# Optimization experiments

Hardware: AMD Instinct MI355X
Metric: run time of the kernel (lower is better)

The kernel has to match this reference:

```python
import jax, jax.numpy as jnp
import numpy as np

N, B, NPG, DEG, F = 16384, 128, 128, 8, 128
E = N * DEG
H1, C1, H2, C2, H3, C3 = 3, 128, 2, 64, 2, 32
D = H1 * C1 + H2 * C2 + C3  # 544
K = 30
ND = 2048
LAMDA = 0.8


def _gatv2(x, src, dst, Wl, Wr, att, b, h, c, concat):
    n = x.shape[0]
    xl = (x @ Wl).reshape(n, h, c)
    xr = (x @ Wr).reshape(n, h, c)
    e = jax.nn.leaky_relu(xl[src] + xr[dst], 0.2)           # [E+N, h, c]
    logit = jnp.einsum('ehc,hc->eh', e, att)
    m = jax.lax.stop_gradient(jax.ops.segment_max(logit, dst, num_segments=n))
    a = jnp.exp(logit - m[dst])
    z = jax.ops.segment_sum(a, dst, num_segments=n)
    a = a / z[dst]
    out = jax.ops.segment_sum(xl[src] * a[:, :, None], dst, num_segments=n)
    out = out.reshape(n, h * c) if concat else out.mean(axis=1)
    return out + b


def _bn(x, g, b):
    m = x.mean(0)
    v = ((x - m) ** 2).mean(0)
    return (x - m) * jax.lax.rsqrt(v + 1e-5) * g + b


def _neighbor(emb, adj, W, b, idx):
    h = emb @ W + b
    A = adj + jnp.eye(adj.shape[0], dtype=adj.dtype)
    d = jax.lax.rsqrt(A.sum(axis=1))
    h = (1.0 - LAMDA) * h + LAMDA * ((d[:, None] * A * d[None, :]) @ h)
    v = h[idx]
    return v / jnp.clip(jnp.linalg.norm(v, axis=1, keepdims=True), 1e-12)


def setup_inputs():
    key = jax.random.key(0)
    it = iter(jax.random.split(key, 48))
    def nrm(shape, s=0.05):
        return jax.random.normal(next(it), shape, jnp.float32) * s
    src = jnp.repeat(jnp.arange(N, dtype=jnp.int32), DEG)
    dst = (src // NPG) * NPG + jax.random.randint(next(it), (E,), 0, NPG, dtype=jnp.int32)
    batch = jnp.arange(N, dtype=jnp.int32) // NPG
    return dict(
        x=jax.random.normal(next(it), (N, F), jnp.float32),
        edge_src=src, edge_dst=dst, batch=batch,
        pairs1=jax.random.randint(next(it), (B,), 0, ND, dtype=jnp.int32),
        pairs2=jax.random.randint(next(it), (B,), 0, ND, dtype=jnp.int32),
        drug_adj=(jax.random.uniform(next(it), (ND, ND)) < 0.01).astype(jnp.float32),
        drug_emb=jax.random.normal(next(it), (ND, ND), jnp.float32) * 0.1,
        dis_adj=(jax.random.uniform(next(it), (ND, ND)) < 0.01).astype(jnp.float32),
        dis_emb=jax.random.normal(next(it), (ND, ND), jnp.float32) * 0.1,
        Wde=nrm((ND, 32)), bde=jnp.zeros((32,), jnp.float32),
        Wse=nrm((ND, 32)), bse=jnp.zeros((32,), jnp.float32),
        W1l=nrm((F, H1 * C1)), W1r=nrm((F, H1 * C1)), att1=nrm((H1, C1)), b1=jnp.zeros((H1 * C1,), jnp.float32),
        W2l=nrm((H1 * C1, H2 * C2)), W2r=nrm((H1 * C1, H2 * C2)), att2=nrm((H2, C2)), b2=jnp.zeros((H2 * C2,), jnp.float32),
        W3l=nrm((H2 * C2, H3 * C3)), W3r=nrm((H2 * C2, H3 * C3)), att3=nrm((H3, C3)), b3=jnp.zeros((C3,), jnp.float32),
        g1=jnp.ones((H1 * C1,), jnp.float32), be1=jnp.zeros((H1 * C1,), jnp.float32),
        g2=jnp.ones((H2 * C2,), jnp.float32), be2=jnp.zeros((H2 * C2,), jnp.float32),
        Ws=nrm((D, K)), bs=jnp.zeros((K,), jnp.float32),
        Wg=nrm((D, D)), bg=jnp.zeros((D,), jnp.float32),
        Wl1=nrm((D * K + 64, 128)), bl1=jnp.zeros((128,), jnp.float32),
        Wl2=nrm((128, 1)), bl2=jnp.zeros((1,), jnp.float32),
    )


def _forward(x, drug_adj, drug_emb, dis_adj, dis_emb, Wde, bde, Wse, bse,
             W1l, W1r, att1, b1, W2l, W2r, att2, b2, W3l, W3r, att3, b3,
             g1, be1, g2, be2, Ws, bs, Wg, bg, Wl1, bl1, Wl2, bl2,
             edge_src, edge_dst, batch, pairs1, pairs2):
    loop = jnp.arange(N, dtype=edge_src.dtype)  # GATv2 self loops
    src = jnp.concatenate([edge_src, loop])
    dst = jnp.concatenate([edge_dst, loop])
    x1 = _bn(jax.nn.relu(_gatv2(x, src, dst, W1l, W1r, att1, b1, H1, C1, True)), g1, be1)
    x2 = _bn(jax.nn.relu(_gatv2(x1, src, dst, W2l, W2r, att2, b2, H2, C2, True)), g2, be2)
    x3 = _gatv2(x2, src, dst, W3l, W3r, att3, b3, H3, C3, False)
    xc = jnp.concatenate([x1, x2, x3], axis=1)              # [N, D]
    xd = xc.reshape(B, NPG, D)                              # to_dense_batch (equal graphs)
    adj = jnp.zeros((B, NPG, NPG), xc.dtype).at[
        batch[edge_src], edge_src % NPG, edge_dst % NPG].add(1.0)
    s = jax.nn.softmax(xd @ Ws + bs, axis=-1)               # [B, NPG, K]
    xp = jnp.einsum('bnk,bnd->bkd', s, xd)                  # pooled features
    ap = jnp.einsum('bnk,bnm,bml->bkl', s, adj, s)          # pooled adjacency
    ap = ap.at[:, jnp.arange(K), jnp.arange(K)].set(1.0)    # DenseGCNConv add_loop
    dg = jax.lax.rsqrt(jnp.clip(ap.sum(-1), 1.0))
    apn = dg[:, :, None] * ap * dg[:, None, :]
    xg = jax.nn.relu(jnp.einsum('bkl,bld->bkd', apn, xp @ Wg) + bg)
    de = _neighbor(drug_emb, drug_adj, Wde, bde, pairs1)    # [B, 32]
    se = _neighbor(dis_emb, dis_adj, Wse, bse, pairs2)      # [B, 32]
    g = jnp.concatenate([de, xg.reshape(B, K * D), se], axis=-1)
    h = jax.nn.relu(g @ Wl1 + bl1)
    return (h @ Wl2 + bl2)[:, 0]


def reference(x, edge_src, edge_dst, batch, pairs1, pairs2, drug_adj, drug_emb, dis_adj, dis_emb,
              Wde, bde, Wse, bse, W1l, W1r, att1, b1, W2l, W2r, att2, b2, W3l, W3r, att3, b3,
              g1, be1, g2, be2, Ws, bs, Wg, bg, Wl1, bl1, Wl2, bl2):
    return _forward(x, drug_adj, drug_emb, dis_adj, dis_emb, Wde, bde, Wse, bse,
                    W1l, W1r, att1, b1, W2l, W2r, att2, b2, W3l, W3r, att3, b3,
                    g1, be1, g2, be2, Ws, bs, Wg, bg, Wl1, bl1, Wl2, bl2,
                    edge_src, edge_dst, batch, pairs1, pairs2)
```

## Files before the change

### kernel.cpp

```cpp
#include <hip/hip_runtime.h>
#include <math.h>

#define CDIV(a,b) (((a)+(b)-1)/(b))
#define HMIN(a,b) ((a)<(b)?(a):(b))
#define MAXD 48

typedef __attribute__((ext_vector_type(8))) short bf16x8;
typedef __attribute__((ext_vector_type(4))) float f32x4;

static __device__ inline short f2bf(float x){
  unsigned u = __float_as_uint(x);
  unsigned r = (u + 0x7fffu + ((u >> 16) & 1u)) >> 16;
  return (short)r;
}

__global__ __launch_bounds__(256)
void transpose_bf16(const float* __restrict__ B, int K, int N, short* __restrict__ Bt)
{
  __shared__ float t[32][33];
  int k0 = blockIdx.x*32, n0 = blockIdx.y*32;
  int c = threadIdx.x & 31, r8 = threadIdx.x >> 5;
  for (int rr = r8; rr < 32; rr += 8) {
    int k = k0+rr, n = n0+c;
    t[rr][c] = (k < K && n < N) ? B[(size_t)k*N + n] : 0.f;
  }
  __syncthreads();
  for (int rr = r8; rr < 32; rr += 8) {
    int n = n0+rr, k = k0+c;
    if (n < N && k < K) Bt[(size_t)n*K + k] = f2bf(t[c][rr]);
  }
}

__global__ __launch_bounds__(256)
void transpose_bf16_2(const float* __restrict__ A0, int K0, int N0, short* __restrict__ D0,
                      const float* __restrict__ A1, int K1, int N1, short* __restrict__ D1)
{
  const float* B; short* Bt; int K, N;
  if (blockIdx.z == 0) { B=A0; Bt=D0; K=K0; N=N0; } else { B=A1; Bt=D1; K=K1; N=N1; }
  int ntx = CDIV(K,32), nty = CDIV(N,32);
  int tile = blockIdx.x;
  if (tile >= ntx*nty) return;
  int k0 = (tile % ntx)*32, n0 = (tile / ntx)*32;
  __shared__ float t[32][33];
  int c = threadIdx.x & 31, r8 = threadIdx.x >> 5;
  for (int rr = r8; rr < 32; rr += 8) {
    int k = k0+rr, n = n0+c;
    t[rr][c] = (k < K && n < N) ? B[(size_t)k*N + n] : 0.f;
  }
  __syncthreads();
  for (int rr = r8; rr < 32; rr += 8) {
    int n = n0+rr, k = k0+c;
    if (n < N && k < K) Bt[(size_t)n*K + k] = f2bf(t[c][rr]);
  }
}

__global__ __launch_bounds__(256)
void gemm_mfma(const float* __restrict__ A, int lda,
               const short* __restrict__ Bt,
               float* __restrict__ C, int ldc,
               int M, int N, int K,
               const float* __restrict__ bias, int relu, int ksplit)
{
  __shared__ short As[128][40];
  __shared__ short Bs[128][40];
  const int k0 = blockIdx.z * ksplit;
  const int k1 = HMIN(k0 + ksplit, K);
  C += (size_t)blockIdx.z * (size_t)M * ldc;
  const int bm = blockIdx.x * 128, bn = blockIdx.y * 128;
  const int tid = threadIdx.x;
  const int sr = tid >> 1;
  const int sk = (tid & 1) * 16;
  const int wave = tid >> 6;
  const int wr = (wave >> 1) * 64, wc = (wave & 1) * 64;
  const int lane = tid & 63;
  const int lrow = lane & 15, lk = (lane >> 4) * 8;

  f32x4 acc[4][4];
  #pragma unroll
  for (int i=0;i<4;i++)
    #pragma unroll
    for (int j=0;j<4;j++) acc[i][j] = (f32x4){0.f,0.f,0.f,0.f};

  const bool bok = (bn + sr) < N;
  for (int kb = k0; kb < k1; kb += 32) {
    __syncthreads();
    {
      const float* ap = A + (size_t)(bm + sr)*lda + kb + sk;
      float4 v0 = *(const float4*)(ap+0);
      float4 v1 = *(const float4*)(ap+4);
      float4 v2 = *(const float4*)(ap+8);
      float4 v3 = *(const float4*)(ap+12);
      bf16x8 w0, w1;
      w0[0]=f2bf(v0.x); w0[1]=f2bf(v0.y); w0[2]=f2bf(v0.z); w0[3]=f2bf(v0.w);
      w0[4]=f2bf(v1.x); w0[5]=f2bf(v1.y); w0[6]=f2bf(v1.z); w0[7]=f2bf(v1.w);
      w1[0]=f2bf(v2.x); w1[1]=f2bf(v2.y); w1[2]=f2bf(v2.z); w1[3]=f2bf(v2.w);
      w1[4]=f2bf(v3.x); w1[5]=f2bf(v3.y); w1[6]=f2bf(v3.z); w1[7]=f2bf(v3.w);
      *(bf16x8*)&As[sr][sk]   = w0;
      *(bf16x8*)&As[sr][sk+8] = w1;
    }
    {
      bf16x8 u0 = (bf16x8){0,0,0,0,0,0,0,0}, u1 = u0;
      if (bok) {
        const short* bp = Bt + (size_t)(bn + sr)*K + kb + sk;
        u0 = *(const bf16x8*)(bp);
        u1 = *(const bf16x8*)(bp+8);
      }
      *(bf16x8*)&Bs[sr][sk]   = u0;
      *(bf16x8*)&Bs[sr][sk+8] = u1;
    }
    __syncthreads();
    bf16x8 af[4], bfr[4];
    #pragma unroll
    for (int f=0;f<4;f++) af[f]  = *(const bf16x8*)&As[wr + f*16 + lrow][lk];
    #pragma unroll
    for (int f=0;f<4;f++) bfr[f] = *(const bf16x8*)&Bs[wc + f*16 + lrow][lk];
    #pragma unroll
    for (int i=0;i<4;i++)
      #pragma unroll
      for (int j=0;j<4;j++)
        acc[i][j] = __builtin_amdgcn_mfma_f32_16x16x32_bf16(af[i], bfr[j], acc[i][j], 0, 0, 0);
  }
  const int erow = (lane >> 4) * 4;
  const int ecol = lane & 15;
  #pragma unroll
  for (int j=0;j<4;j++) {
    int gcol = bn + wc + j*16 + ecol;
    if (gcol >= N) continue;
    float bv = bias ? bias[gcol] : 0.f;
    #pragma unroll
    for (int i=0;i<4;i++) {
      int grow = bm + wr + i*16 + erow;
      #pragma unroll
      for (int r=0;r<4;r++) {
        float v = acc[i][j][r] + bv;
        if (relu) v = fmaxf(v, 0.f);
        C[(size_t)(grow + r)*ldc + gcol] = v;
      }
    }
  }
}

__global__ __launch_bounds__(256)
void skinny_gemm32(const float* __restrict__ A, int lda,
                   const float* __restrict__ B,
                   float* __restrict__ Cp, int M, int ksplit)
{
  const int m0 = blockIdx.x * 32;
  const int k0 = blockIdx.z * ksplit;
  __shared__ float As[32][68];
  __shared__ float Bs[64][36];
  float acc[4] = {0.f,0.f,0.f,0.f};
  const int r  = threadIdx.x >> 3;
  const int cg = (threadIdx.x & 7) * 4;
  for (int kb = k0; kb < k0 + ksplit; kb += 64) {
    {
      int rr = threadIdx.x >> 3, ko = (threadIdx.x & 7)*8;
      const float* ap = &A[(size_t)(m0+rr)*lda + kb + ko];
      *(float4*)&As[rr][ko]   = *(const float4*)ap;
      *(float4*)&As[rr][ko+4] = *(const float4*)(ap+4);
      int br = threadIdx.x >> 2, co = (threadIdx.x & 3)*8;
      const float* bp = &B[(size_t)(kb+br)*32 + co];
      *(float4*)&Bs[br][co]   = *(const float4*)bp;
      *(float4*)&Bs[br][co+4] = *(const float4*)(bp+4);
    }
    __syncthreads();
    #pragma unroll
    for (int kk=0; kk<64; kk+=4) {
      float4 a4 = *(const float4*)&As[r][kk];
      float4 b0 = *(const float4*)&Bs[kk  ][cg];
      float4 b1 = *(const float4*)&Bs[kk+1][cg];
      float4 b2 = *(const float4*)&Bs[kk+2][cg];
      float4 b3 = *(const float4*)&Bs[kk+3][cg];
      acc[0] += a4.x*b0.x + a4.y*b1.x + a4.z*b2.x + a4.w*b3.x;
      acc[1] += a4.x*b0.y + a4.y*b1.y + a4.z*b2.y + a4.w*b3.y;
      acc[2] += a4.x*b0.z + a4.y*b1.z + a4.z*b2.z + a4.w*b3.z;
      acc[3] += a4.x*b0.w + a4.y*b1.w + a4.z*b2.w + a4.w*b3.w;
    }
    __syncthreads();
  }
  float* cp = Cp + ((size_t)blockIdx.z*M + m0 + r)*32 + cg;
  *(float4*)cp = make_float4(acc[0],acc[1],acc[2],acc[3]);
}

__global__ void build_adj(const int* __restrict__ src, const int* __restrict__ dst,
                          int E, float* __restrict__ adj)
{
  int e = blockIdx.x*blockDim.x + threadIdx.x;
  if (e >= E) return;
  int s = src[e], d = dst[e];
  int g = s >> 7;
  atomicAdd(&adj[((size_t)g*128 + (s & 127))*128 + (d & 127)], 1.0f);
}

__global__ __launch_bounds__(1024)
void build_nbr(const int* __restrict__ dst, int epg, int shift,
               int* __restrict__ nbr, int* __restrict__ deg)
{
  __shared__ short ld[1024];
  const int g = blockIdx.x;
  for (int i = threadIdx.x; i < epg; i += 1024) ld[i] = (short)(dst[g*epg + i] & 127);
  __syncthreads();
  const int d   = threadIdx.x >> 3;
  const int seg = threadIdx.x & 7;
  const int spe = epg >> 3;
  const int i0 = seg*spe, i1 = i0 + spe;
  int cnt = 0;
  for (int i = i0; i < i1; ++i) cnt += (ld[i] == (short)d) ? 1 : 0;
  int pre = cnt;
  #pragma unroll
  for (int off=1; off<8; off<<=1) {
    int v = __shfl_up(pre, off, 8);
    if (seg >= off) pre += v;
  }
  const int base  = pre - cnt;
  const int total = __shfl(pre, 7, 8);
  if (seg == 7) deg[g*128 + d] = HMIN(total, MAXD);
  const int lbase = (g*128 + d)*MAXD;
  int w = base;
  for (int i = i0; i < i1; ++i) {
    if (ld[i] == (short)d) {
      if (w < MAXD) nbr[lbase + w] = i >> shift;
      ++w;
    }
  }
}

template<int C, int NL>
__global__ __launch_bounds__(512)
void gat_attn_sp(const float* __restrict__ XL, const float* __restrict__ XR, int ldx,
                 const float* __restrict__ att,
                 const int* __restrict__ nbr, const int* __restrict__ deg,
                 const float* __restrict__ bias, int bias_per_head,
                 float* __restrict__ out, int ldo)
{
  constexpr int SPAN = C / NL;
  constexpr int NG = 512 / NL;
  constexpr int PADC = C + 4;
  __shared__ float xls[128][PADC];
  __shared__ float A_lds[128];
  __shared__ float lgs[NG][MAXD+4];
  const int g = blockIdx.x, hh = blockIdx.y;
  const int d0 = blockIdx.z * 64;
  const int colbase = hh*C;
  const int tid = threadIdx.x;
  const int lane = tid & (NL-1);
  const int grp  = tid / NL;

  for (int idx = tid; idx < 128*(C/4); idx += 512) {
    int r = idx / (C/4), q4 = idx % (C/4);
    *(float4*)&xls[r][q4*4] =
      *(const float4*)&XL[(size_t)(g*128+r)*ldx + colbase + q4*4];
  }
  float attv[SPAN];
  #pragma unroll
  for (int j=0;j<SPAN;j++) attv[j] = att[hh*C + lane*SPAN + j];
  __syncthreads();

  for (int s = grp; s < 128; s += NG) {
    float a = 0.f;
    #pragma unroll
    for (int j4=0;j4<SPAN;j4+=4) {
      float4 xv = *(const float4*)&xls[s][lane*SPAN + j4];
      a += attv[j4+0]*xv.x + attv[j4+1]*xv.y + attv[j4+2]*xv.z + attv[j4+3]*xv.w;
    }
    #pragma unroll
    for (int t=1;t<NL;t<<=1) a += __shfl_xor(a, t, 64);
    if (lane == 0) A_lds[s] = a;
  }
  __syncthreads();

  for (int d = d0 + grp; d < d0 + 64; d += NG) {
    float xrv[SPAN];
    #pragma unroll
    for (int j4=0;j4<SPAN;j4+=4)
      *(float4*)&xrv[j4] =
        *(const float4*)&XR[(size_t)(g*128+d)*ldx + colbase + lane*SPAN + j4];
    float B = 0.f;
    #pragma unroll
    for (int j=0;j<SPAN;j++) B += attv[j]*xrv[j];
    #pragma unroll
    for (int t=1;t<NL;t<<=1) B += __shfl_xor(B, t, 64);
    const int dgn = deg[g*128+d];
    const int base = (g*128+d)*MAXD;
    float m = -1e30f;
    for (int i = 0; i <= dgn; ++i) {
      int s = (i < dgn) ? nbr[base+i] : d;
      float dot = 0.f;
      #pragma unroll
      for (int j4=0;j4<SPAN;j4+=4) {
        float4 xv = *(const float4*)&xls[s][lane*SPAN + j4];
        dot += attv[j4+0]*fabsf(xv.x + xrv[j4+0]);
        dot += attv[j4+1]*fabsf(xv.y + xrv[j4+1]);
        dot += attv[j4+2]*fabsf(xv.z + xrv[j4+2]);
        dot += attv[j4+3]*fabsf(xv.w + xrv[j4+3]);
      }
      #pragma unroll
      for (int t=1;t<NL;t<<=1) dot += __shfl_xor(dot, t, 64);
      float lg = 0.6f*(A_lds[s] + B) + 0.4f*dot;
      if (lane == 0) lgs[grp][i] = lg;
      m = fmaxf(m, lg);
    }
    float z = 0.f;
    for (int i = lane; i <= dgn; i += NL) z += __expf(lgs[grp][i] - m);
    #pragma unroll
    for (int t=1;t<NL;t<<=1) z += __shfl_xor(z, t, 64);
    const float zinv = 1.f / z;
    for (int i = lane; i <= dgn; i += NL) lgs[grp][i] = __expf(lgs[grp][i] - m) * zinv;
    float acc[SPAN];
    #pragma unroll
    for (int j=0;j<SPAN;j++) acc[j]=0.f;
    for (int i = 0; i <= dgn; ++i) {
      int s = (i < dgn) ? nbr[base+i] : d;
      float P = lgs[grp][i];
      #pragma unroll
      for (int j4=0;j4<SPAN;j4+=4) {
        float4 xv = *(const float4*)&xls[s][lane*SPAN + j4];
        acc[j4+0] += P*xv.x; acc[j4+1] += P*xv.y;
        acc[j4+2] += P*xv.z; acc[j4+3] += P*xv.w;
      }
    }
    float o[SPAN];
    #pragma unroll
    for (int j=0;j<SPAN;j++) {
      int cc = lane*SPAN + j;
      float bv = bias ? (bias_per_head ? bias[colbase+cc] : bias[cc]) : 0.f;
      o[j] = acc[j] + bv;
    }
    float* op = &out[(size_t)(g*128+d)*ldo + colbase + lane*SPAN];
    #pragma unroll
    for (int j4=0;j4<SPAN;j4+=4)
      *(float4*)&op[j4] = make_float4(o[j4],o[j4+1],o[j4+2],o[j4+3]);
  }
}

__global__ __launch_bounds__(256)
void bn_partial(const float* __restrict__ in, int HC,
                float* __restrict__ psum, float* __restrict__ psq)
{
  const int cg = blockIdx.x, rb = blockIdx.y;
  const int cl = threadIdx.x & 31;
  const int rl = threadIdx.x >> 5;
  const int col = cg*32 + cl;
  float s = 0.f, s2 = 0.f;
  for (int r = rb*512 + rl; r < (rb+1)*512; r += 8) {
    float v = fmaxf(in[(size_t)r*HC + col], 0.f);
    s += v; s2 += v*v;
  }
  __shared__ float ls[8][33], ls2[8][33];
  ls[rl][cl] = s; ls2[rl][cl] = s2;
  __syncthreads();
  if (threadIdx.x < 32) {
    float a=0.f, a2=0.f;
    for (int r=0;r<8;r++){ a += ls[r][threadIdx.x]; a2 += ls2[r][threadIdx.x]; }
    psum[rb*HC + cg*32 + threadIdx.x] = a;
    psq [rb*HC + cg*32 + threadIdx.x] = a2;
  }
}

__global__ void bn_finalize(const float* __restrict__ psum, const float* __restrict__ psq,
                            int HC, float* __restrict__ mv)
{
  int c = blockIdx.x*blockDim.x + threadIdx.x;
  if (c >= HC) return;
  float s=0.f, s2=0.f;
  for (int r=0;r<32;r++){ s += psum[r*HC+c]; s2 += psq[r*HC+c]; }
  float m = s * (1.f/16384.f);
  float v = s2 * (1.f/16384.f) - m*m;
  mv[c] = m; mv[HC+c] = v;
}

__global__ void bn_apply(const float* __restrict__ in, int HC,
                         const float* __restrict__ mv,
                         const float* __restrict__ gamma, const float* __restrict__ beta,
                         float* __restrict__ out, int ldo, int total)
{
  int i = blockIdx.x*blockDim.x + threadIdx.x;
  if (i >= total) return;
  int r = i / HC, c = i % HC;
  float v = fmaxf(in[i], 0.f);
  out[(size_t)r*ldo + c] = (v - mv[c]) * rsqrtf(mv[HC+c] + 1e-5f) * gamma[c] + beta[c];
}

__global__ void combine3(const float* __restrict__ raw, float* __restrict__ xc)
{
  int i = blockIdx.x*blockDim.x + threadIdx.x;
  if (i >= 16384*32) return;
  int r = i >> 5, c = i & 31;
  xc[(size_t)r*544 + 512 + c] = 0.5f*(raw[r*64 + c] + raw[r*64 + 32 + c]);
}

__global__ void softmax30(float* __restrict__ s, int M)
{
  int w = (blockIdx.x*blockDim.x + threadIdx.x) >> 5;
  int lane = threadIdx.x & 31;
  if (w >= M) return;
  float v = (lane < 30) ? s[(size_t)w*30 + lane] : -1e30f;
  float m = v;
  for (int t=16;t>0;t>>=1) m = fmaxf(m, __shfl_xor(m, t, 32));
  float e = (lane < 30) ? __expf(v - m) : 0.f;
  float z = e;
  for (int t=16;t>0;t>>=1) z += __shfl_xor(z, t, 32);
  if (lane < 30) s[(size_t)w*30 + lane] = e / z;
}

__global__ __launch_bounds__(256)
void xp_kernel(const float* __restrict__ s, const float* __restrict__ xc,
               float* __restrict__ xp)
{
  const int b = blockIdx.x;
  const int d = blockIdx.y*256 + threadIdx.x;
  __shared__ float sb[128][32];
  for (int idx = threadIdx.x; idx < 128*30; idx += 256) {
    int n = idx/30, k = idx%30;
    sb[n][k] = s[(size_t)(b*128+n)*30 + k];
  }
  __syncthreads();
  if (d >= 544) return;
  float acc[30];
  #pragma unroll
  for (int k=0;k<30;k++) acc[k]=0.f;
  const float* xcp = xc + (size_t)b*128*544 + d;
  for (int n=0;n<128;n++) {
    float xcv = xcp[(size_t)n*544];
    const float4* sp = (const float4*)&sb[n][0];
    #pragma unroll
    for (int q=0;q<7;q++) {
      float4 v = sp[q];
      acc[q*4+0] += v.x*xcv; acc[q*4+1] += v.y*xcv;
      acc[q*4+2] += v.z*xcv; acc[q*4+3] += v.w*xcv;
    }
    float2 v2 = *(const float2*)&sb[n][28];
    acc[28] += v2.x*xcv; acc[29] += v2.y*xcv;
  }
  #pragma unroll
  for (int k=0;k<30;k++) xp[((size_t)b*30+k)*544 + d] = acc[k];
}

__global__ __launch_bounds__(256)
void pool_adj_kernel(const float* __restrict__ adj, const float* __restrict__ s,
                     float* __restrict__ apn)
{
  const int b = blockIdx.x;
  __shared__ float sb[128][32];
  __shared__ float t1s[128][32];
  __shared__ float apb[30][31];
  __shared__ float dg[30];
  for (int idx = threadIdx.x; idx < 128*30; idx += 256) {
    int n = idx/30, k = idx%30;
    sb[n][k] = s[(size_t)(b*128+n)*30 + k];
  }
  __syncthreads();
  if (threadIdx.x < 128) {
    const int i = threadIdx.x;
    float acc[30];
    #pragma unroll
    for (int k=0;k<30;k++) acc[k]=0.f;
    const float* arow = adj + ((size_t)b*128 + i)*128;
    for (int j=0;j<128;j++) {
      float a = arow[j];
      const float4* sp = (const float4*)&sb[j][0];
      #pragma unroll
      for (int q=0;q<7;q++) {
        float4 v = sp[q];
        acc[q*4+0] += v.x*a; acc[q*4+1] += v.y*a;
        acc[q*4+2] += v.z*a; acc[q*4+3] += v.w*a;
      }
      float2 v2 = *(const float2*)&sb[j][28];
      acc[28] += v2.x*a; acc[29] += v2.y*a;
    }
    #pragma unroll
    for (int k=0;k<30;k++) t1s[i][k] = acc[k];
  }
  __syncthreads();
  for (int idx = threadIdx.x; idx < 900; idx += 256) {
    int k = idx/30, l = idx%30;
    float acc = 0.f;
    for (int n=0;n<128;n++) acc += sb[n][k]*t1s[n][l];
    apb[k][l] = (k == l) ? 1.f : acc;
  }
  __syncthreads();
  if (threadIdx.x < 30) {
    float ssum = 0.f;
    for (int l=0;l<30;l++) ssum += apb[threadIdx.x][l];
    dg[threadIdx.x] = rsqrtf(fmaxf(ssum, 1.f));
  }
  __syncthreads();
  for (int idx = threadIdx.x; idx < 900; idx += 256) {
    int k = idx/30, l = idx%30;
    apn[(size_t)b*900 + idx] = dg[k]*dg[l]*apb[k][l];
  }
}

__global__ __launch_bounds__(256)
void xg_kernel(const float* __restrict__ apn, const float* __restrict__ xpw,
               const float* __restrict__ bg, float* __restrict__ g)
{
  int b = blockIdx.x;
  __shared__ float a[30][31];
  for (int idx = threadIdx.x; idx < 900; idx += 256)
    a[idx/30][idx%30] = apn[(size_t)b*900 + idx];
  __syncthreads();
  for (int idx = threadIdx.x; idx < 30*544; idx += 256) {
    int k = idx / 544, d = idx % 544;
    float acc = 0.f;
    for (int l=0;l<30;l++) acc += a[k][l] * xpw[((size_t)b*30 + l)*544 + d];
    g[(size_t)b*16384 + 32 + k*544 + d] = fmaxf(acc + bg[d], 0.f);
  }
}

__global__ __launch_bounds__(256)
void rowsum_rsqrt(const float* __restrict__ A, int n, float* __restrict__ dinv)
{
  int r = blockIdx.x;
  float s = 0.f;
  for (int j = threadIdx.x; j < n; j += 256) s += A[(size_t)r*n + j];
  for (int m=32;m>0;m>>=1) s += __shfl_xor(s, m, 64);
  __shared__ float red[4];
  if ((threadIdx.x & 63) == 0) red[threadIdx.x >> 6] = s;
  __syncthreads();
  if (threadIdx.x == 0) dinv[r] = rsqrtf(red[0]+red[1]+red[2]+red[3] + 1.f);
}

__global__ __launch_bounds__(256)
void embed_partial(const float* __restrict__ adjM, const float* __restrict__ hW,
                   const float* __restrict__ dinv, const int* __restrict__ idx,
                   float* __restrict__ part)
{
  const int b = blockIdx.x;
  const int z = blockIdx.z;
  const int row = idx[b];
  const int c  = threadIdx.x & 31;
  const int jc = threadIdx.x >> 5;
  const int j0 = z*64;
  float u = 0.f;
  #pragma unroll
  for (int t=0;t<8;t++) {
    int j = j0 + jc + t*8;
    u += adjM[(size_t)row*2048 + j] * hW[j*32 + c] * dinv[j];
  }
  __shared__ float red[8][33];
  red[jc][c] = u;
  __syncthreads();
  if (threadIdx.x < 32) {
    float s = 0.f;
    #pragma unroll
    for (int r=0;r<8;r++) s += red[r][threadIdx.x];
    part[((size_t)z*128 + b)*32 + threadIdx.x] = s;
  }
}

__global__ void embed_final(const float* __restrict__ part, const float* __restrict__ hW,
                            const float* __restrict__ dinv, const int* __restrict__ idx,
                            float* __restrict__ g, int goff)
{
  const int b = blockIdx.x;
  const int c = threadIdx.x;
  const int row = idx[b];
  float s = 0.f;
  for (int z=0; z<32; ++z) s += part[((size_t)z*128 + b)*32 + c];
  float hw = hW[(size_t)row*32 + c];
  float dv = dinv[row];
  float h2 = 0.2f*hw + 0.8f*dv*(s + hw*dv);
  float ss = h2*h2;
  #pragma unroll
  for (int m=1;m<32;m<<=1) ss += __shfl_xor(ss, m, 32);
  float nrm = fmaxf(sqrtf(ss), 1e-12f);
  g[(size_t)b*16384 + goff + c] = h2 / nrm;
}

__global__ void reduce_parts(const float* __restrict__ part, const float* __restrict__ bias,
                             float* __restrict__ outp, int total, int nz, int ldc, int relu)
{
  int i = blockIdx.x*blockDim.x + threadIdx.x;
  if (i >= total) return;
  float s = 0.f;
  for (int p=0;p<nz;p++) s += part[(size_t)p*total + i];
  if (bias) s += bias[i % ldc];
  if (relu) s = fmaxf(s, 0.f);
  outp[i] = s;
}

__global__ void final_out(const float* __restrict__ h, const float* __restrict__ Wl2,
                          const float* __restrict__ bl2, float* __restrict__ out)
{
  int m = threadIdx.x;
  if (m >= 128) return;
  float s = 0.f;
  for (int k=0;k<128;k++) s += h[m*128 + k] * Wl2[k];
  out[m] = s + bl2[0];
}

extern "C" void kernel_launch(void* const* d_in, const int* in_sizes, int n_in,
                              void* d_out, int out_size, void* d_ws, size_t ws_size,
                              hipStream_t stream)
{
  const float* x        = (const float*)d_in[0];
  const int*   edge_src = (const int*)d_in[1];
  const int*   edge_dst = (const int*)d_in[2];
  const int*   pairs1   = (const int*)d_in[4];
  const int*   pairs2   = (const int*)d_in[5];
  const float* drug_adj = (const float*)d_in[6];
  const float* drug_emb = (const float*)d_in[7];
  const float* dis_adj  = (const float*)d_in[8];
  const float* dis_emb  = (const float*)d_in[9];
  const float* Wde = (const float*)d_in[10];
  const float* bde = (const float*)d_in[11];
  const float* Wse = (const float*)d_in[12];
  const float* bse = (const float*)d_in[13];
  const float* W1l = (const float*)d_in[14];
  const float* W1r = (const float*)d_in[15];
  const float* att1= (const float*)d_in[16];
  const float* b1  = (const float*)d_in[17];
  const float* W2l = (const float*)d_in[18];
  const float* W2r = (const float*)d_in[19];
  const float* att2= (const float*)d_in[20];
  const float* b2  = (const float*)d_in[21];
  const float* W3l = (const float*)d_in[22];
  const float* W3r = (const float*)d_in[23];
  const float* att3= (const float*)d_in[24];
  const float* b3  = (const float*)d_in[25];
  const float* g1  = (const float*)d_in[26];
  const float* be1 = (const float*)d_in[27];
  const float* g2  = (const float*)d_in[28];
  const float* be2 = (const float*)d_in[29];
  const float* Wsm = (const float*)d_in[30];
  const float* bs  = (const float*)d_in[31];
  const float* Wg  = (const float*)d_in[32];
  const float* bg  = (const float*)d_in[33];
  const float* Wl1 = (const float*)d_in[34];
  const float* bl1 = (const float*)d_in[35];
  const float* Wl2 = (const float*)d_in[36];
  const float* bl2 = (const float*)d_in[37];
  float* out = (float*)d_out;

  const int E = in_sizes[1];
  const int epg = E >> 7;
  const int shift = 31 - __builtin_clz(epg >> 7);

  float* ws  = (float*)d_ws;
  float* adj = ws;
  int*   nbr = (int*)adj;
  int*   degb= nbr + 16384*MAXD;
  float* xc  = ws + 2097152;
  float* P   = ws + 11010048;
  float* XLR = P;
  float* RAW = P + 12582912;
  float* bnp = ws + 29884416;
  float* bnq = bnp + 12288;
  float* mv  = bnq + 12288;
  short* wT  = (short*)(mv + 1024);
  float* sbuf = P;
  float* xp   = P + 491520;
  float* apn  = P + 3187200;
  float* xpw  = P + 3302400;
  float* gbuf = P + 5391360;
  float* hWd  = P + 7488512;
  float* dinvd= hWd + 65536;
  float* hWs_ = dinvd + 2048;
  float* dinvs= hWs_ + 65536;
  float* upart= dinvs + 2048;
  float* partials = upart + 131072;
  float* hfin = partials + 1048576;
  float* epart = hfin + 16384;
  short* wgT  = (short*)epart;
  short* wl1T = (short*)RAW;

  build_nbr<<<128, 1024, 0, stream>>>(edge_dst, epg, shift, nbr, degb);

  transpose_bf16_2<<<dim3(48,1,2), 256, 0, stream>>>(W1l, 128, 384, wT,
                                                     W1r, 128, 384, wT + 384*128);
  gemm_mfma<<<dim3(128,6,1), 256, 0, stream>>>(x, 128, wT, XLR, 768, 16384, 768, 128, nullptr, 0, 128);
  gat_attn_sp<128,16><<<dim3(128,3,2), 512, 0, stream>>>(XLR, XLR + 384, 768, att1, nbr, degb, b1, 1, RAW, 384);
  bn_partial<<<dim3(12,32), 256, 0, stream>>>(RAW, 384, bnp, bnq);
  bn_finalize<<<2, 256, 0, stream>>>(bnp, bnq, 384, mv);
  bn_apply<<<CDIV(16384*384,256), 256, 0, stream>>>(RAW, 384, mv, g1, be1, xc, 544, 16384*384);

  transpose_bf16_2<<<dim3(48,1,2), 256, 0, stream>>>(W2l, 384, 128, wT,
                                                     W2r, 384, 128, wT + 128*384);
  gemm_mfma<<<dim3(128,2,1), 256, 0, stream>>>(xc, 544, wT, XLR, 256, 16384, 256, 384, nullptr, 0, 384);
  gat_attn_sp<64,8><<<dim3(128,2,2), 512, 0, stream>>>(XLR, XLR + 128, 256, att2, nbr, degb, b2, 1, RAW, 128);
  bn_partial<<<dim3(4,32), 256, 0, stream>>>(RAW, 128, bnp, bnq);
  bn_finalize<<<1, 256, 0, stream>>>(bnp, bnq, 128, mv);
  bn_apply<<<CDIV(16384*128,256), 256, 0, stream>>>(RAW, 128, mv, g2, be2, xc + 384, 544, 16384*128);

  transpose_bf16_2<<<dim3(8,1,2), 256, 0, stream>>>(W3l, 128, 64, wT,
                                                    W3r, 128, 64, wT + 64*128);
  gemm_mfma<<<dim3(128,1,1), 256, 0, stream>>>(xc + 384, 544, wT, XLR, 128, 16384, 128, 128, nullptr, 0, 128);
  gat_attn_sp<32,8><<<dim3(128,2,2), 512, 0, stream>>>(XLR, XLR + 64, 128, att3, nbr, degb, b3, 0, RAW, 64);
  combine3<<<CDIV(16384*32,256), 256, 0, stream>>>(RAW, xc);

  hipMemsetAsync(adj, 0, (size_t)2097152*4, stream);
  build_adj<<<CDIV(E,256), 256, 0, stream>>>(edge_src, edge_dst, E, adj);

  transpose_bf16_2<<<dim3(289,1,2), 256, 0, stream>>>(Wsm, 544, 30, wT,
                                                      Wg, 544, 544, wgT);
  gemm_mfma<<<dim3(128,1,1), 256, 0, stream>>>(xc, 544, wT, sbuf, 30, 16384, 30, 544, bs, 0, 544);
  softmax30<<<CDIV(16384*32,256), 256, 0, stream>>>(sbuf, 16384);
  xp_kernel<<<dim3(128,3), 256, 0, stream>>>(sbuf, xc, xp);
  pool_adj_kernel<<<128, 256, 0, stream>>>(adj, sbuf, apn);
  gemm_mfma<<<dim3(30,5,1), 256, 0, stream>>>(xp, 544, wgT, xpw, 544, 3840, 544, 544, nullptr, 0, 544);
  xg_kernel<<<128, 256, 0, stream>>>(apn, xpw, bg, gbuf);

  skinny_gemm32<<<dim3(64,1,8), 256, 0, stream>>>(drug_emb, 2048, Wde, epart, 2048, 256);
  reduce_parts<<<CDIV(65536,256), 256, 0, stream>>>(epart, bde, hWd, 65536, 8, 32, 0);
  rowsum_rsqrt<<<2048, 256, 0, stream>>>(drug_adj, 2048, dinvd);
  embed_partial<<<dim3(128,1,32), 256, 0, stream>>>(drug_adj, hWd, dinvd, pairs1, upart);
  embed_final<<<128, 32, 0, stream>>>(upart, hWd, dinvd, pairs1, gbuf, 0);

  skinny_gemm32<<<dim3(64,1,8), 256, 0, stream>>>(dis_emb, 2048, Wse, epart, 2048, 256);
  reduce_parts<<<CDIV(65536,256), 256, 0, stream>>>(epart, bse, hWs_, 65536, 8, 32, 0);
  rowsum_rsqrt<<<2048, 256, 0, stream>>>(dis_adj, 2048, dinvs);
  embed_partial<<<dim3(128,1,32), 256, 0, stream>>>(dis_adj, hWs_, dinvs, pairs2, upart);
  embed_final<<<128, 32, 0, stream>>>(upart, hWs_, dinvs, pairs2, gbuf, 16352);

  transpose_bf16<<<dim3(512,4), 256, 0, stream>>>(Wl1, 16384, 128, wl1T);
  gemm_mfma<<<dim3(1,1,32), 256, 0, stream>>>(gbuf, 16384, wl1T, partials, 128, 128, 128, 16384, nullptr, 0, 512);
  reduce_parts<<<CDIV(16384,256), 256, 0, stream>>>(partials, bl1, hfin, 16384, 32, 128, 1);
  final_out<<<1, 128, 0, stream>>>(hfin, Wl2, bl2, out);
}
```

Measured before the change: 485.8 us.

## Store GAT source features as bf16 in LDS, vectorize BN apply, deepen split-K

The GAT attention kernel now keeps its staged XL tile in shared memory as bf16 instead of fp32. This halves LDS footprint and read bandwidth, at some cost in numeric precision. The BN apply kernel is rewritten to process four elements per thread with float4 loads and stores. The final large-K GEMM split goes from 32 to 64 partitions, which adds parallelism but makes the partial buffer and reduction larger.

```diff
diff --git a/kernel.cpp b/kernel.cpp
--- a/kernel.cpp
+++ b/kernel.cpp
@@ -12,6 +12,9 @@
   unsigned u = __float_as_uint(x);
   unsigned r = (u + 0x7fffu + ((u >> 16) & 1u)) >> 16;
   return (short)r;
+}
+static __device__ inline float bf2f(short s){
+  return __uint_as_float(((unsigned)(unsigned short)s) << 16);
 }
 
 __global__ __launch_bounds__(256)
@@ -235,8 +238,8 @@
 {
   constexpr int SPAN = C / NL;
   constexpr int NG = 512 / NL;
-  constexpr int PADC = C + 4;
-  __shared__ float xls[128][PADC];
+  constexpr int PADC = C + 8;
+  __shared__ short xls[128][PADC];
   __shared__ float A_lds[128];
   __shared__ float lgs[NG][MAXD+4];
   const int g = blockIdx.x, hh = blockIdx.y;
@@ -246,10 +249,12 @@
   const int lane = tid & (NL-1);
   const int grp  = tid / NL;
 
-  for (int idx = tid; idx < 128*(C/4); idx += 512) {
+  for (int idx = tid; idx < 128*C/4; idx += 512) {
     int r = idx / (C/4), q4 = idx % (C/4);
-    *(float4*)&xls[r][q4*4] =
-      *(const float4*)&XL[(size_t)(g*128+r)*ldx + colbase + q4*4];
+    float4 v = *(const float4*)&XL[(size_t)(g*128+r)*ldx + colbase + q4*4];
+    short4 w;
+    w.x = f2bf(v.x); w.y = f2bf(v.y); w.z = f2bf(v.z); w.w = f2bf(v.w);
+    *(short4*)&xls[r][q4*4] = w;
   }
   float attv[SPAN];
   #pragma unroll
@@ -260,8 +265,9 @@
     float a = 0.f;
     #pragma unroll
     for (int j4=0;j4<SPAN;j4+=4) {
-      float4 xv = *(const float4*)&xls[s][lane*SPAN + j4];
-      a += attv[j4+0]*xv.x + attv[j4+1]*xv.y + attv[j4+2]*xv.z + attv[j4+3]*xv.w;
+      short4 xv = *(const short4*)&xls[s][lane*SPAN + j4];
+      a += attv[j4+0]*bf2f(xv.x) + attv[j4+1]*bf2f(xv.y)
+         + attv[j4+2]*bf2f(xv.z) + attv[j4+3]*bf2f(xv.w);
     }
     #pragma unroll
     for (int t=1;t<NL;t<<=1) a += __shfl_xor(a, t, 64);
@@ -272,9 +278,7 @@
   for (int d = d0 + grp; d < d0 + 64; d += NG) {
     float xrv[SPAN];
     #pragma unroll
-    for (int j4=0;j4<SPAN;j4+=4)
-      *(float4*)&xrv[j4] =
-        *(const float4*)&XR[(size_t)(g*128+d)*ldx + colbase + lane*SPAN + j4];
+    for (int j=0;j<SPAN;j++) xrv[j] = XR[(size_t)(g*128+d)*ldx + colbase + lane*SPAN + j];
     float B = 0.f;
     #pragma unroll
     for (int j=0;j<SPAN;j++) B += attv[j]*xrv[j];
@@ -288,11 +292,11 @@
       float dot = 0.f;
       #pragma unroll
       for (int j4=0;j4<SPAN;j4+=4) {
-        float4 xv = *(const float4*)&xls[s][lane*SPAN + j4];
-        dot += attv[j4+0]*fabsf(xv.x + xrv[j4+0]);
-        dot += attv[j4+1]*fabsf(xv.y + xrv[j4+1]);
-        dot += attv[j4+2]*fabsf(xv.z + xrv[j4+2]);
-        dot += attv[j4+3]*fabsf(xv.w + xrv[j4+3]);
+        short4 xv = *(const short4*)&xls[s][lane*SPAN + j4];
+        dot += attv[j4+0]*fabsf(bf2f(xv.x) + xrv[j4+0]);
+        dot += attv[j4+1]*fabsf(bf2f(xv.y) + xrv[j4+1]);
+        dot += attv[j4+2]*fabsf(bf2f(xv.z) + xrv[j4+2]);
+        dot += attv[j4+3]*fabsf(bf2f(xv.w) + xrv[j4+3]);
       }
       #pragma unroll
       for (int t=1;t<NL;t<<=1) dot += __shfl_xor(dot, t, 64);
@@ -314,9 +318,9 @@
       float P = lgs[grp][i];
       #pragma unroll
       for (int j4=0;j4<SPAN;j4+=4) {
-        float4 xv = *(const float4*)&xls[s][lane*SPAN + j4];
-        acc[j4+0] += P*xv.x; acc[j4+1] += P*xv.y;
-        acc[j4+2] += P*xv.z; acc[j4+3] += P*xv.w;
+        short4 xv = *(const short4*)&xls[s][lane*SPAN + j4];
+        acc[j4+0] += P*bf2f(xv.x); acc[j4+1] += P*bf2f(xv.y);
+        acc[j4+2] += P*bf2f(xv.z); acc[j4+3] += P*bf2f(xv.w);
       }
     }
     float o[SPAN];
@@ -369,16 +373,26 @@
   mv[c] = m; mv[HC+c] = v;
 }
 
-__global__ void bn_apply(const float* __restrict__ in, int HC,
-                         const float* __restrict__ mv,
-                         const float* __restrict__ gamma, const float* __restrict__ beta,
-                         float* __restrict__ out, int ldo, int total)
-{
-  int i = blockIdx.x*blockDim.x + threadIdx.x;
-  if (i >= total) return;
+__global__ void bn_apply4(const float* __restrict__ in, int HC,
+                          const float* __restrict__ mv,
+                          const float* __restrict__ gamma, const float* __restrict__ beta,
+                          float* __restrict__ out, int ldo, int total4)
+{
+  int i4 = blockIdx.x*blockDim.x + threadIdx.x;
+  if (i4 >= total4) return;
+  size_t i = (size_t)i4*4;
   int r = i / HC, c = i % HC;
-  float v = fmaxf(in[i], 0.f);
-  out[(size_t)r*ldo + c] = (v - mv[c]) * rsqrtf(mv[HC+c] + 1e-5f) * gamma[c] + beta[c];
+  float4 v = *(const float4*)&in[i];
+  float4 mvv = *(const float4*)&mv[c];
+  float4 vav = *(const float4*)&mv[HC+c];
+  float4 gv = *(const float4*)&gamma[c];
+  float4 bv = *(const float4*)&beta[c];
+  float4 o;
+  o.x = (fmaxf(v.x,0.f) - mvv.x) * rsqrtf(vav.x + 1e-5f) * gv.x + bv.x;
+  o.y = (fmaxf(v.y,0.f) - mvv.y) * rsqrtf(vav.y + 1e-5f) * gv.y + bv.y;
+  o.z = (fmaxf(v.z,0.f) - mvv.z) * rsqrtf(vav.z + 1e-5f) * gv.z + bv.z;
+  o.w = (fmaxf(v.w,0.f) - mvv.w) * rsqrtf(vav.w + 1e-5f) * gv.w + bv.w;
+  *(float4*)&out[(size_t)r*ldo + c] = o;
 }
 
 __global__ void combine3(const float* __restrict__ raw, float* __restrict__ xc)
@@ -673,7 +687,7 @@
   gat_attn_sp<128,16><<<dim3(128,3,2), 512, 0, stream>>>(XLR, XLR + 384, 768, att1, nbr, degb, b1, 1, RAW, 384);
   bn_partial<<<dim3(12,32), 256, 0, stream>>>(RAW, 384, bnp, bnq);
   bn_finalize<<<2, 256, 0, stream>>>(bnp, bnq, 384, mv);
-  bn_apply<<<CDIV(16384*384,256), 256, 0, stream>>>(RAW, 384, mv, g1, be1, xc, 544, 16384*384);
+  bn_apply4<<<CDIV(16384*96,256), 256, 0, stream>>>(RAW, 384, mv, g1, be1, xc, 544, 16384*96);
 
   transpose_bf16_2<<<dim3(48,1,2), 256, 0, stream>>>(W2l, 384, 128, wT,
                                                      W2r, 384, 128, wT + 128*384);
@@ -681,7 +695,7 @@
   gat_attn_sp<64,8><<<dim3(128,2,2), 512, 0, stream>>>(XLR, XLR + 128, 256, att2, nbr, degb, b2, 1, RAW, 128);
   bn_partial<<<dim3(4,32), 256, 0, stream>>>(RAW, 128, bnp, bnq);
   bn_finalize<<<1, 256, 0, stream>>>(bnp, bnq, 128, mv);
-  bn_apply<<<CDIV(16384*128,256), 256, 0, stream>>>(RAW, 128, mv, g2, be2, xc + 384, 544, 16384*128);
+  bn_apply4<<<CDIV(16384*32,256), 256, 0, stream>>>(RAW, 128, mv, g2, be2, xc + 384, 544, 16384*32);
 
   transpose_bf16_2<<<dim3(8,1,2), 256, 0, stream>>>(W3l, 128, 64, wT,
                                                     W3r, 128, 64, wT + 64*128);
@@ -714,7 +728,7 @@
   embed_final<<<128, 32, 0, stream>>>(upart, hWs_, dinvs, pairs2, gbuf, 16352);
 
   transpose_bf16<<<dim3(512,4), 256, 0, stream>>>(Wl1, 16384, 128, wl1T);
-  gemm_mfma<<<dim3(1,1,32), 256, 0, stream>>>(gbuf, 16384, wl1T, partials, 128, 128, 128, 16384, nullptr, 0, 512);
-  reduce_parts<<<CDIV(16384,256), 256, 0, stream>>>(partials, bl1, hfin, 16384, 32, 128, 1);
+  gemm_mfma<<<dim3(1,1,64), 256, 0, stream>>>(gbuf, 16384, wl1T, partials, 128, 128, 128, 16384, nullptr, 0, 256);
+  reduce_parts<<<CDIV(16384,256), 256, 0, stream>>>(partials, bl1, hfin, 16384, 64, 128, 1);
   final_out<<<1, 128, 0, stream>>>(hfin, Wl2, bl2, out);
 }
```

New measurement: 462.6 us. -4.8%, faster.
